# Kernel optimization log

Measured on AMD Instinct MI355X. Metric: run time of the kernel, lower is better.

Reference implementation:

```python
import jax, jax.numpy as jnp
import numpy as np

B, N, F_IN = 32, 512, 16
H, D_HID, D_OUT = 8, 8, 32
ALPHA = 0.2
NEG = -9e15


def setup_inputs() -> dict:
    key = jax.random.key(0)
    ks = jax.random.split(key, 10)
    xv = jax.random.normal(ks[0], (B, N, F_IN), dtype=jnp.float32)
    adj = (jax.random.uniform(ks[1], (B, N, N)) < 0.05).astype(jnp.float32)
    s = 0.1
    W_heads = jax.random.normal(ks[2], (H, F_IN, D_HID), dtype=jnp.float32) * s
    a1 = jax.random.normal(ks[3], (H, D_HID), dtype=jnp.float32) * s
    a2 = jax.random.normal(ks[4], (H, D_HID), dtype=jnp.float32) * s
    W_out = jax.random.normal(ks[5], (H * D_HID, D_OUT), dtype=jnp.float32) * s
    a1_out = jax.random.normal(ks[6], (D_OUT,), dtype=jnp.float32) * s
    a2_out = jax.random.normal(ks[7], (D_OUT,), dtype=jnp.float32) * s
    W_q = jax.random.normal(ks[8], (N * D_OUT, N), dtype=jnp.float32) * s
    b_q = jax.random.normal(ks[9], (N,), dtype=jnp.float32) * s
    return {"xv": xv, "adj": adj, "W_heads": W_heads, "a1": a1, "a2": a2,
            "W_out": W_out, "a1_out": a1_out, "a2_out": a2_out,
            "W_q": W_q, "b_q": b_q}


def _masked_softmax(e, adj_mask):
    # e: [..., N, N]; adj_mask broadcastable bool
    scores = jnp.where(adj_mask, e, NEG)
    return jax.nn.softmax(scores, axis=-1)


def reference(xv, adj, W_heads, a1, a2, W_out, a1_out, a2_out, W_q, b_q):
    mask = adj > 0  # [B, N, N]
    # --- multi-head GAT layer (vectorized over batch and heads) ---
    Wh = jnp.einsum('bnf,hfd->bhnd', xv, W_heads)            # [B,H,N,Dh]
    f1 = jnp.einsum('bhnd,hd->bhn', Wh, a1)                   # a^T[:Dh] . Wh_i
    f2 = jnp.einsum('bhnd,hd->bhn', Wh, a2)                   # a^T[Dh:] . Wh_j
    e = jax.nn.leaky_relu(f1[:, :, :, None] + f2[:, :, None, :], ALPHA)  # [B,H,N,N]
    att = _masked_softmax(e, mask[:, None, :, :])
    h = jnp.einsum('bhnm,bhmd->bhnd', att, Wh)
    h = jax.nn.elu(h)                                         # concat=True heads apply elu
    h_cat = jnp.transpose(h, (0, 2, 1, 3)).reshape(B, N, H * D_HID)  # head-major concat
    # --- output attention layer (concat=False: no internal elu) ---
    Who = jnp.einsum('bnf,fd->bnd', h_cat, W_out)             # [B,N,Do]
    g1 = Who @ a1_out                                         # [B,N]
    g2 = Who @ a2_out
    eo = jax.nn.leaky_relu(g1[:, :, None] + g2[:, None, :], ALPHA)
    att_o = _masked_softmax(eo, mask)
    out = jnp.einsum('bnm,bmd->bnd', att_o, Who)
    out = jax.nn.elu(out)                                     # F.elu applied in forward
    # --- Q head ---
    q = out.reshape(B, N * D_OUT) @ W_q + b_q                 # [B,N]
    return q[..., None]                                       # [B,N,1]
```

## Files before the change

### kernel.cpp

```cpp
#include <hip/hip_runtime.h>
#include <stdint.h>


typedef unsigned long long u64;
typedef unsigned short u16;

__device__ __forceinline__ float eluf(float x) { return x > 0.f ? x : __expf(x) - 1.f; }
__device__ __forceinline__ float lrelu(float x) { return fmaxf(x, 0.2f * x); }

__device__ __align__(16) u64   g_mask[131072];
__device__ __align__(16) float g_whg[1048576];
__device__ __align__(16) float g_f1[131072];
__device__ __align__(16) float g_f2[131072];
__device__ __align__(16) float g_Who[524288];
__device__ __align__(16) float g_g1[16384];
__device__ __align__(16) float g_g2[16384];
__device__ __align__(16) float g_out2[524288];
__device__ __align__(16) float g_partial[2097152];

__global__ __launch_bounds__(512) void k_wh(const float* __restrict__ xv,
                                            const float* __restrict__ whd,
                                            const float* __restrict__ a1,
                                            const float* __restrict__ a2) {
  const int bid = blockIdx.x;
  const int b = bid & 31;
  const int o = bid >> 5;
  const int tid = threadIdx.x;
  const int h = __builtin_amdgcn_readfirstlane(tid >> 6);
  const int col = o * 64 + (tid & 63);

  const float4* xp = (const float4*)(xv + ((size_t)b * 512 + col) * 16);
  float x[16];
#pragma unroll
  for (int i = 0; i < 4; ++i) {
    float4 v = xp[i];
    x[4 * i] = v.x; x[4 * i + 1] = v.y; x[4 * i + 2] = v.z; x[4 * i + 3] = v.w;
  }
  const float* Wr = whd + h * 128;
  float wh[8] = {0, 0, 0, 0, 0, 0, 0, 0};
#pragma unroll
  for (int f = 0; f < 16; ++f) {
    float xf = x[f];
#pragma unroll
    for (int d = 0; d < 8; ++d) wh[d] += xf * Wr[f * 8 + d];
  }
  float s1 = 0.f, s2 = 0.f;
#pragma unroll
  for (int d = 0; d < 8; ++d) { s1 += wh[d] * a1[h * 8 + d]; s2 += wh[d] * a2[h * 8 + d]; }

  float* dst = g_whg + (((size_t)b * 512 + col) * 8 + h) * 8;
  *(float4*)dst = make_float4(wh[0], wh[1], wh[2], wh[3]);
  *(float4*)(dst + 4) = make_float4(wh[4], wh[5], wh[6], wh[7]);
  g_f1[((size_t)b * 512 + col) * 8 + h] = s1;
  g_f2[((size_t)b * 512 + col) * 8 + h] = s2;
}

__global__ __launch_bounds__(512) void k_gat(const float* __restrict__ adj,
                                             const float* __restrict__ wout,
                                             const float* __restrict__ a1o,
                                             const float* __restrict__ a2o) {
  __shared__ u16 list[32 * 64];
  __shared__ int cnt[32];
  __shared__ __align__(16) float wout_s[2048];
  __shared__ float a1os[32], a2os[32];
  __shared__ __align__(16) float hcat[32 * 68];

  const int bid = blockIdx.x;
  const int b = bid & 31;
  const int c0 = bid >> 5;
  const int tid = threadIdx.x;
  const int wv = tid >> 6, l = tid & 63;

  for (int i = tid; i < 2048; i += 512) wout_s[i] = wout[i];
  if (tid < 32) { a1os[tid] = a1o[tid]; a2os[tid] = a2o[tid]; }

#pragma unroll 1
  for (int rr = 0; rr < 4; ++rr) {
    int row_l = wv * 4 + rr;
    int row_g = c0 * 32 + row_l;
    const float* ap = adj + ((size_t)b * 512 + row_g) * 512 + l;
    float v[8];
#pragma unroll
    for (int s = 0; s < 8; ++s) v[s] = ap[s * 64];
    int base = 0;
#pragma unroll
    for (int s = 0; s < 8; ++s) {
      u64 bal = __ballot(v[s] > 0.f);
      if (l == 0) g_mask[(size_t)b * 4096 + (size_t)row_g * 8 + s] = bal;
      if (v[s] > 0.f) {
        int idx = base + __popcll(bal & ((1ull << l) - 1ull));
        if (idx < 64) list[row_l * 64 + idx] = (u16)(s * 64 + l);
      }
      base += __popcll(bal);
    }
    if (l == 0) cnt[row_l] = base < 64 ? base : 64;
  }
  __syncthreads();

  const int row_l = tid >> 4, h = (tid >> 1) & 7, half = tid & 1;
  const int row_g = c0 * 32 + row_l;
  float acc[8] = {0, 0, 0, 0, 0, 0, 0, 0};
  float sum = 0.f;
  {
    const int n = cnt[row_l];
    const float f1v = g_f1[((size_t)b * 512 + row_g) * 8 + h];
    const float* whb = g_whg + (size_t)b * 32768;
    const float* f2b = g_f2 + (size_t)b * 4096;
    for (int e = half; e < n; e += 2) {
      int col = (int)list[row_l * 64 + e];
      float p = __expf(lrelu(f1v + f2b[col * 8 + h]));
      sum += p;
      const float4* wp = (const float4*)(whb + (size_t)(col * 8 + h) * 8);
      float4 A = wp[0], Bv = wp[1];
      acc[0] += p * A.x;  acc[1] += p * A.y;  acc[2] += p * A.z;  acc[3] += p * A.w;
      acc[4] += p * Bv.x; acc[5] += p * Bv.y; acc[6] += p * Bv.z; acc[7] += p * Bv.w;
    }
  }
#pragma unroll
  for (int d = 0; d < 8; ++d) acc[d] += __shfl_xor(acc[d], 1);
  sum += __shfl_xor(sum, 1);

  if (half == 0) {
    float rs = sum > 0.f ? 1.0f / sum : 0.f;
    *(float4*)&hcat[row_l * 68 + h * 8] =
        make_float4(eluf(acc[0] * rs), eluf(acc[1] * rs), eluf(acc[2] * rs), eluf(acc[3] * rs));
    *(float4*)&hcat[row_l * 68 + h * 8 + 4] =
        make_float4(eluf(acc[4] * rs), eluf(acc[5] * rs), eluf(acc[6] * rs), eluf(acc[7] * rs));
  }
  __syncthreads();

  {
    const int row = tid >> 4, sub = tid & 15, kh = sub >> 3, dq = (sub & 7) * 4;
    const float* hrow = &hcat[row * 68 + kh * 32];
    float a4[4] = {0, 0, 0, 0};
#pragma unroll
    for (int k4 = 0; k4 < 8; ++k4) {
      float4 h4 = *(const float4*)&hrow[k4 * 4];
      float hv[4] = {h4.x, h4.y, h4.z, h4.w};
#pragma unroll
      for (int j = 0; j < 4; ++j) {
        float4 w4 = *(const float4*)&wout_s[(kh * 32 + k4 * 4 + j) * 32 + dq];
        a4[0] += hv[j] * w4.x; a4[1] += hv[j] * w4.y;
        a4[2] += hv[j] * w4.z; a4[3] += hv[j] * w4.w;
      }
    }
#pragma unroll
    for (int j = 0; j < 4; ++j) a4[j] += __shfl_xor(a4[j], 8);
    float s1 = a4[0] * a1os[dq] + a4[1] * a1os[dq + 1] +
               a4[2] * a1os[dq + 2] + a4[3] * a1os[dq + 3];
    float s2 = a4[0] * a2os[dq] + a4[1] * a2os[dq + 1] +
               a4[2] * a2os[dq + 2] + a4[3] * a2os[dq + 3];
    s1 += __shfl_xor(s1, 1); s1 += __shfl_xor(s1, 2); s1 += __shfl_xor(s1, 4);
    s2 += __shfl_xor(s2, 1); s2 += __shfl_xor(s2, 2); s2 += __shfl_xor(s2, 4);
    size_t g = (size_t)b * 512 + row_g;
    if (kh == 0) *(float4*)(g_Who + g * 32 + dq) = make_float4(a4[0], a4[1], a4[2], a4[3]);
    if (sub == 0) { g_g1[g] = s1; g_g2[g] = s2; }
  }
}

__global__ __launch_bounds__(1024) void k_att2() {
  extern __shared__ float lds2[];
  constexpr int POOL = 0;
  constexpr int G2C = 18432;
  constexpr int MASKS = 18944;

  const int bid = blockIdx.x;
  const int b = bid & 31;
  const int t = bid >> 5;
  const int tid = threadIdx.x;
  const int w = tid >> 6, l = tid & 63;
  u64* mask_s = (u64*)&lds2[MASKS];

  if (tid < 512) mask_s[tid] = g_mask[(size_t)b * 4096 + t * 512 + tid];
  if (tid < 128) ((float4*)&lds2[G2C])[tid] = ((const float4*)g_g2)[(size_t)b * 128 + tid];
  {
    const float4* src = (const float4*)g_Who + (size_t)b * 4096;
    for (int i = tid; i < 4096; i += 1024) {
      int m = i >> 3, d4 = i & 7;
      *(float4*)&lds2[POOL + m * 36 + d4 * 4] = src[i];
    }
  }
  float g1v = g_g1[(size_t)b * 512 + t * 64 + l];
  __syncthreads();

  float acc[32];
#pragma unroll
  for (int d = 0; d < 32; ++d) acc[d] = 0.f;
  float sum = 0.f;
  {
    const int c = w >> 3, wc = w & 7;
    u64 mq = mask_s[l * 8 + c * 4 + (wc >> 1)];
    uint32_t bits = (wc & 1) ? (uint32_t)(mq >> 32) : (uint32_t)mq;
    while (bits) {
      int j = __builtin_ctz(bits);
      bits &= bits - 1;
      int col = c * 256 + wc * 32 + j;
      float p = __expf(lrelu(g1v + lds2[G2C + col]));
      sum += p;
      const float* wq = &lds2[POOL + col * 36];
#pragma unroll
      for (int d4 = 0; d4 < 8; ++d4) {
        float4 v = *(const float4*)(wq + d4 * 4);
        acc[d4 * 4]     += p * v.x;
        acc[d4 * 4 + 1] += p * v.y;
        acc[d4 * 4 + 2] += p * v.z;
        acc[d4 * 4 + 3] += p * v.w;
      }
    }
  }

#pragma unroll 1
  for (int step = 8; step >= 1; step >>= 1) {
    __syncthreads();
    if (w >= step && w < 2 * step) {
      float* rp = &lds2[POOL + (size_t)((w - step) * 64 + l) * 36];
#pragma unroll
      for (int d4 = 0; d4 < 8; ++d4)
        *(float4*)(rp + d4 * 4) = make_float4(acc[d4 * 4], acc[d4 * 4 + 1], acc[d4 * 4 + 2], acc[d4 * 4 + 3]);
      rp[32] = sum;
    }
    __syncthreads();
    if (w < step) {
      const float* rp = &lds2[POOL + (size_t)(w * 64 + l) * 36];
#pragma unroll
      for (int d = 0; d < 32; ++d) acc[d] += rp[d];
      sum += rp[32];
    }
  }

  if (w == 0) {
    float rs = sum > 0.f ? 1.0f / sum : 0.f;
    float* dst = g_out2 + (size_t)(b * 512 + t * 64 + l) * 32;
#pragma unroll
    for (int d4 = 0; d4 < 8; ++d4)
      *(float4*)(dst + d4 * 4) = make_float4(eluf(acc[d4 * 4] * rs), eluf(acc[d4 * 4 + 1] * rs),
                                             eluf(acc[d4 * 4 + 2] * rs), eluf(acc[d4 * 4 + 3] * rs));
  }
}

__global__ __launch_bounds__(512) void k_qpart(const float* __restrict__ Wq) {
  __shared__ __align__(16) float outS[4608];
  int s = blockIdx.x >> 1;
  int c = blockIdx.x & 1;
  int tid = threadIdx.x;
  int lane = tid & 63;
  int bg = tid >> 6;

  {
    int bb = tid >> 4;
    int kk8 = (tid & 15) * 8;
    const float* src = g_out2 + (size_t)bb * 16384 + s * 128 + kk8;
    float4 v0 = *(const float4*)src;
    float4 v1 = *(const float4*)(src + 4);
    outS[(kk8 + 0) * 36 + bb] = v0.x; outS[(kk8 + 1) * 36 + bb] = v0.y;
    outS[(kk8 + 2) * 36 + bb] = v0.z; outS[(kk8 + 3) * 36 + bb] = v0.w;
    outS[(kk8 + 4) * 36 + bb] = v1.x; outS[(kk8 + 5) * 36 + bb] = v1.y;
    outS[(kk8 + 6) * 36 + bb] = v1.z; outS[(kk8 + 7) * 36 + bb] = v1.w;
  }
  __syncthreads();

  const float* wp = Wq + (size_t)(s * 128) * 512 + c * 256 + lane * 4;
  float4 acc4[4];
#pragma unroll
  for (int j = 0; j < 4; ++j) acc4[j] = make_float4(0.f, 0.f, 0.f, 0.f);

#pragma unroll 8
  for (int kk = 0; kk < 128; ++kk) {
    float4 wv4 = *(const float4*)(wp + (size_t)kk * 512);
    const float* ob = outS + kk * 36 + bg * 4;
    float4 o = *(const float4*)ob;
    float ov[4] = {o.x, o.y, o.z, o.w};
#pragma unroll
    for (int j = 0; j < 4; ++j) {
      acc4[j].x += ov[j] * wv4.x; acc4[j].y += ov[j] * wv4.y;
      acc4[j].z += ov[j] * wv4.z; acc4[j].w += ov[j] * wv4.w;
    }
  }
#pragma unroll
  for (int j = 0; j < 4; ++j)
    *(float4*)(g_partial + (size_t)(s * 32 + bg * 4 + j) * 512 + c * 256 + lane * 4) = acc4[j];
}

__global__ __launch_bounds__(512) void k_qred(const float* __restrict__ bq,
                                              float* __restrict__ out) {
  __shared__ float red[512];
  int tid = threadIdx.x;
  int w = tid >> 6, l = tid & 63;
  int g = blockIdx.x * 64 + l;
  int b = g >> 9, np = g & 511;
  float q = 0.f;
#pragma unroll
  for (int i = 0; i < 16; ++i) {
    int s = w + i * 8;
    q += g_partial[(size_t)(s * 32 + b) * 512 + np];
  }
  red[w * 64 + l] = q;
  __syncthreads();
  if (w == 0) {
    float tacc = bq[np];
#pragma unroll
    for (int k = 0; k < 8; ++k) tacc += red[k * 64 + l];
    out[g] = tacc;
  }
}

extern "C" void kernel_launch(void* const* d_in, const int* in_sizes, int n_in,
                              void* d_out, int out_size, void* d_ws, size_t ws_size,
                              hipStream_t stream) {
  const float* xv = (const float*)d_in[0];
  const float* adj = (const float*)d_in[1];
  const float* W_heads = (const float*)d_in[2];
  const float* a1 = (const float*)d_in[3];
  const float* a2 = (const float*)d_in[4];
  const float* W_out = (const float*)d_in[5];
  const float* a1_out = (const float*)d_in[6];
  const float* a2_out = (const float*)d_in[7];
  const float* W_q = (const float*)d_in[8];
  const float* b_q = (const float*)d_in[9];

  static bool inited = false;
  if (!inited) {
    hipFuncSetAttribute(reinterpret_cast<const void*>(k_att2),
                        hipFuncAttributeMaxDynamicSharedMemorySize, 79872);
    inited = true;
  }

  k_wh<<<256, 512, 0, stream>>>(xv, W_heads, a1, a2);
  k_gat<<<512, 512, 0, stream>>>(adj, W_out, a1_out, a2_out);
  k_att2<<<256, 1024, 79872, stream>>>();
  k_qpart<<<256, 512, 0, stream>>>(W_q);
  k_qred<<<256, 512, 0, stream>>>(b_q, (float*)d_out);
}
```

Measured before the change: 161.3 us.

## Relayout head-major Wh/f buffers, shrink k_gat blocks, prefetch W_q in att2

Stores Wh, f1 and f2 head-major per batch so each head's gather reads a contiguous per-head slab. k_gat drops from 32 rows per 512-thread block to 8 rows per 256-thread block, with four lanes per row/head splitting the neighbour list, giving more, smaller blocks. Idle waves in k_att2 now load the W_q slice that k_qpart will use next and discard it, to warm the cache before that kernel runs. The prefetch adds memory traffic and extra work inside att2, which could slow that kernel.

```diff
diff --git a/kernel.cpp b/kernel.cpp
--- a/kernel.cpp
+++ b/kernel.cpp
@@ -48,36 +48,36 @@
 #pragma unroll
   for (int d = 0; d < 8; ++d) { s1 += wh[d] * a1[h * 8 + d]; s2 += wh[d] * a2[h * 8 + d]; }
 
-  float* dst = g_whg + (((size_t)b * 512 + col) * 8 + h) * 8;
+  float* dst = g_whg + ((size_t)b * 8 + h) * 4096 + (size_t)col * 8;
   *(float4*)dst = make_float4(wh[0], wh[1], wh[2], wh[3]);
   *(float4*)(dst + 4) = make_float4(wh[4], wh[5], wh[6], wh[7]);
-  g_f1[((size_t)b * 512 + col) * 8 + h] = s1;
-  g_f2[((size_t)b * 512 + col) * 8 + h] = s2;
-}
-
-__global__ __launch_bounds__(512) void k_gat(const float* __restrict__ adj,
+  g_f1[((size_t)b * 8 + h) * 512 + col] = s1;
+  g_f2[((size_t)b * 8 + h) * 512 + col] = s2;
+}
+
+__global__ __launch_bounds__(256) void k_gat(const float* __restrict__ adj,
                                              const float* __restrict__ wout,
                                              const float* __restrict__ a1o,
                                              const float* __restrict__ a2o) {
-  __shared__ u16 list[32 * 64];
-  __shared__ int cnt[32];
+  __shared__ u16 list[8 * 64];
+  __shared__ int cnt[8];
   __shared__ __align__(16) float wout_s[2048];
   __shared__ float a1os[32], a2os[32];
-  __shared__ __align__(16) float hcat[32 * 68];
+  __shared__ __align__(16) float hcat[8 * 68];
 
   const int bid = blockIdx.x;
   const int b = bid & 31;
-  const int c0 = bid >> 5;
+  const int ch = bid >> 5;
   const int tid = threadIdx.x;
   const int wv = tid >> 6, l = tid & 63;
 
-  for (int i = tid; i < 2048; i += 512) wout_s[i] = wout[i];
+  for (int i = tid; i < 2048; i += 256) wout_s[i] = wout[i];
   if (tid < 32) { a1os[tid] = a1o[tid]; a2os[tid] = a2o[tid]; }
 
-#pragma unroll 1
-  for (int rr = 0; rr < 4; ++rr) {
-    int row_l = wv * 4 + rr;
-    int row_g = c0 * 32 + row_l;
+#pragma unroll
+  for (int rr = 0; rr < 2; ++rr) {
+    int row_l = wv * 2 + rr;
+    int row_g = ch * 8 + row_l;
     const float* ap = adj + ((size_t)b * 512 + row_g) * 512 + l;
     float v[8];
 #pragma unroll
@@ -97,55 +97,63 @@
   }
   __syncthreads();
 
-  const int row_l = tid >> 4, h = (tid >> 1) & 7, half = tid & 1;
-  const int row_g = c0 * 32 + row_l;
-  float acc[8] = {0, 0, 0, 0, 0, 0, 0, 0};
-  float sum = 0.f;
-  {
+  {
+    const int row_l = tid >> 5, h = (tid >> 2) & 7, q = tid & 3;
+    const int row_g = ch * 8 + row_l;
+    float acc[8] = {0, 0, 0, 0, 0, 0, 0, 0};
+    float sum = 0.f;
     const int n = cnt[row_l];
-    const float f1v = g_f1[((size_t)b * 512 + row_g) * 8 + h];
-    const float* whb = g_whg + (size_t)b * 32768;
-    const float* f2b = g_f2 + (size_t)b * 4096;
-    for (int e = half; e < n; e += 2) {
+    const float f1v = g_f1[((size_t)b * 8 + h) * 512 + row_g];
+    const float* whb = g_whg + ((size_t)b * 8 + h) * 4096;
+    const float* f2b = g_f2 + ((size_t)b * 8 + h) * 512;
+    for (int e = q; e < n; e += 4) {
       int col = (int)list[row_l * 64 + e];
-      float p = __expf(lrelu(f1v + f2b[col * 8 + h]));
+      float p = __expf(lrelu(f1v + f2b[col]));
       sum += p;
-      const float4* wp = (const float4*)(whb + (size_t)(col * 8 + h) * 8);
+      const float4* wp = (const float4*)(whb + (size_t)col * 8);
       float4 A = wp[0], Bv = wp[1];
       acc[0] += p * A.x;  acc[1] += p * A.y;  acc[2] += p * A.z;  acc[3] += p * A.w;
       acc[4] += p * Bv.x; acc[5] += p * Bv.y; acc[6] += p * Bv.z; acc[7] += p * Bv.w;
     }
-  }
-#pragma unroll
-  for (int d = 0; d < 8; ++d) acc[d] += __shfl_xor(acc[d], 1);
-  sum += __shfl_xor(sum, 1);
-
-  if (half == 0) {
-    float rs = sum > 0.f ? 1.0f / sum : 0.f;
-    *(float4*)&hcat[row_l * 68 + h * 8] =
-        make_float4(eluf(acc[0] * rs), eluf(acc[1] * rs), eluf(acc[2] * rs), eluf(acc[3] * rs));
-    *(float4*)&hcat[row_l * 68 + h * 8 + 4] =
-        make_float4(eluf(acc[4] * rs), eluf(acc[5] * rs), eluf(acc[6] * rs), eluf(acc[7] * rs));
-  }
-  __syncthreads();
-
-  {
-    const int row = tid >> 4, sub = tid & 15, kh = sub >> 3, dq = (sub & 7) * 4;
-    const float* hrow = &hcat[row * 68 + kh * 32];
+#pragma unroll
+    for (int d = 0; d < 8; ++d) {
+      acc[d] += __shfl_xor(acc[d], 1);
+      acc[d] += __shfl_xor(acc[d], 2);
+    }
+    sum += __shfl_xor(sum, 1);
+    sum += __shfl_xor(sum, 2);
+
+    if (q == 0) {
+      float rs = sum > 0.f ? 1.0f / sum : 0.f;
+      *(float4*)&hcat[row_l * 68 + h * 8] =
+          make_float4(eluf(acc[0] * rs), eluf(acc[1] * rs), eluf(acc[2] * rs), eluf(acc[3] * rs));
+      *(float4*)&hcat[row_l * 68 + h * 8 + 4] =
+          make_float4(eluf(acc[4] * rs), eluf(acc[5] * rs), eluf(acc[6] * rs), eluf(acc[7] * rs));
+    }
+  }
+  __syncthreads();
+
+  {
+    const int row = tid >> 5, sub = tid & 31, kq = sub >> 3, dq = (sub & 7) * 4;
+    const int row_g = ch * 8 + row;
+    const float* hrow = &hcat[row * 68 + kq * 16];
     float a4[4] = {0, 0, 0, 0};
 #pragma unroll
-    for (int k4 = 0; k4 < 8; ++k4) {
+    for (int k4 = 0; k4 < 4; ++k4) {
       float4 h4 = *(const float4*)&hrow[k4 * 4];
       float hv[4] = {h4.x, h4.y, h4.z, h4.w};
 #pragma unroll
       for (int j = 0; j < 4; ++j) {
-        float4 w4 = *(const float4*)&wout_s[(kh * 32 + k4 * 4 + j) * 32 + dq];
+        float4 w4 = *(const float4*)&wout_s[(kq * 16 + k4 * 4 + j) * 32 + dq];
         a4[0] += hv[j] * w4.x; a4[1] += hv[j] * w4.y;
         a4[2] += hv[j] * w4.z; a4[3] += hv[j] * w4.w;
       }
     }
 #pragma unroll
-    for (int j = 0; j < 4; ++j) a4[j] += __shfl_xor(a4[j], 8);
+    for (int j = 0; j < 4; ++j) {
+      a4[j] += __shfl_xor(a4[j], 8);
+      a4[j] += __shfl_xor(a4[j], 16);
+    }
     float s1 = a4[0] * a1os[dq] + a4[1] * a1os[dq + 1] +
                a4[2] * a1os[dq + 2] + a4[3] * a1os[dq + 3];
     float s2 = a4[0] * a2os[dq] + a4[1] * a2os[dq + 1] +
@@ -153,12 +161,12 @@
     s1 += __shfl_xor(s1, 1); s1 += __shfl_xor(s1, 2); s1 += __shfl_xor(s1, 4);
     s2 += __shfl_xor(s2, 1); s2 += __shfl_xor(s2, 2); s2 += __shfl_xor(s2, 4);
     size_t g = (size_t)b * 512 + row_g;
-    if (kh == 0) *(float4*)(g_Who + g * 32 + dq) = make_float4(a4[0], a4[1], a4[2], a4[3]);
+    if (kq == 0) *(float4*)(g_Who + g * 32 + dq) = make_float4(a4[0], a4[1], a4[2], a4[3]);
     if (sub == 0) { g_g1[g] = s1; g_g2[g] = s2; }
   }
 }
 
-__global__ __launch_bounds__(1024) void k_att2() {
+__global__ __launch_bounds__(1024) void k_att2(const float* __restrict__ Wq) {
   extern __shared__ float lds2[];
   constexpr int POOL = 0;
   constexpr int G2C = 18432;
@@ -235,6 +243,15 @@
     for (int d4 = 0; d4 < 8; ++d4)
       *(float4*)(dst + d4 * 4) = make_float4(eluf(acc[d4 * 4] * rs), eluf(acc[d4 * 4 + 1] * rs),
                                              eluf(acc[d4 * 4 + 2] * rs), eluf(acc[d4 * 4 + 3] * rs));
+  } else {
+    const int s = bid >> 1, c = bid & 1;
+    const float4* wq4 = (const float4*)(Wq + (size_t)s * 128 * 512 + c * 256);
+#pragma unroll 1
+    for (int k = tid - 64; k < 8192; k += 960) {
+      int r = k >> 6, cc = k & 63;
+      float4 v = wq4[(size_t)r * 128 + cc];
+      asm volatile("" :: "v"(v.x), "v"(v.y), "v"(v.z), "v"(v.w));
+    }
   }
 }
 
@@ -326,8 +343,8 @@
   }
 
   k_wh<<<256, 512, 0, stream>>>(xv, W_heads, a1, a2);
-  k_gat<<<512, 512, 0, stream>>>(adj, W_out, a1_out, a2_out);
-  k_att2<<<256, 1024, 79872, stream>>>();
+  k_gat<<<2048, 256, 0, stream>>>(adj, W_out, a1_out, a2_out);
+  k_att2<<<256, 1024, 79872, stream>>>(W_q);
   k_qpart<<<256, 512, 0, stream>>>(W_q);
   k_qred<<<256, 512, 0, stream>>>(b_q, (float*)d_out);
 }
```

New measurement: 171.0 us. 6.1% more time.
